# Kernel optimization log

Hardware: AMD Instinct MI355X
Metric: run time of the kernel (lower is better)

## Reference

```python
import jax, jax.numpy as jnp
import numpy as np

N_NODES = 50000
N_EDGES = 800000
NFEAT, NHID, ZDIM = 256, 128, 32
N_PAIRS = 10000


def spmm(row, col, val, h, n):
    # sparse adj (COO) @ dense h : gather source rows, scale, segment-sum into dest rows
    return jax.ops.segment_sum(val[:, None] * h[col], row, num_segments=n)


def setup_inputs() -> dict:
    key = jax.random.key(0)
    ks = jax.random.split(key, 16)
    features = jax.random.normal(ks[0], (N_NODES, NFEAT), dtype=jnp.float32)
    adj_row = jnp.sort(jax.random.randint(ks[1], (N_EDGES,), 0, N_NODES, dtype=jnp.int32))
    adj_col = jax.random.randint(ks[2], (N_EDGES,), 0, N_NODES, dtype=jnp.int32)
    adj_val = jax.random.uniform(ks[3], (N_EDGES,), dtype=jnp.float32)
    idx = jax.random.randint(ks[4], (2, N_PAIRS), 0, N_NODES, dtype=jnp.int32)
    sc = lambda fan: 1.0 / np.sqrt(fan)
    W0 = jax.random.normal(ks[5], (NFEAT, NHID), dtype=jnp.float32) * sc(NFEAT)
    b0 = jnp.zeros((NHID,), jnp.float32)
    W1 = jax.random.normal(ks[6], (NHID, NHID), dtype=jnp.float32) * sc(NHID)
    b1 = jnp.zeros((NHID,), jnp.float32)
    W2 = jax.random.normal(ks[7], (NHID, NHID), dtype=jnp.float32) * sc(NHID)
    b2 = jnp.zeros((NHID,), jnp.float32)
    bil_w = jax.random.normal(ks[8], (ZDIM, NHID, NHID), dtype=jnp.float32) * sc(NHID)
    bil_b = jnp.zeros((ZDIM,), jnp.float32)
    dw1 = jax.random.normal(ks[9], (ZDIM, ZDIM), dtype=jnp.float32) * sc(ZDIM)
    db1 = jnp.zeros((ZDIM,), jnp.float32)
    dw2 = jax.random.normal(ks[10], (ZDIM, 1), dtype=jnp.float32) * sc(ZDIM)
    db2 = jnp.zeros((1,), jnp.float32)
    return dict(features=features, adj_row=adj_row, adj_col=adj_col, adj_val=adj_val,
                idx=idx, W0=W0, b0=b0, W1=W1, b1=b1, W2=W2, b2=b2,
                bil_w=bil_w, bil_b=bil_b, dw1=dw1, db1=db1, dw2=dw2, db2=db2)


def reference(features, adj_row, adj_col, adj_val, idx,
              W0, b0, W1, b1, W2, b2, bil_w, bil_b, dw1, db1, dw2, db2):
    n = features.shape[0]
    # encode: stacked GCN layers (Kipf: relu(adj @ (x @ W) + b)), residual from layer 1 on
    x = jax.nn.relu(spmm(adj_row, adj_col, adj_val, features @ W0, n) + b0)
    res = x
    x = jax.nn.relu(spmm(adj_row, adj_col, adj_val, x @ W1, n) + b1) + res
    res = x
    x = jax.nn.relu(spmm(adj_row, adj_col, adj_val, x @ W2, n) + b2) + res
    latent = x  # dropout p=0.0 -> identity
    # decode: bilinear on node pairs, ELU, 2-layer MLP
    a = latent[idx[0]]  # [P, NHID]
    b = latent[idx[1]]  # [P, NHID]
    feat = jax.nn.elu(jnp.einsum('pd,kde,pe->pk', a, bil_w, b) + bil_b)
    h = jax.nn.elu(feat @ dw1 + db1)
    predictions = h @ dw2 + db2  # [P, 1]
    return predictions, latent
```

## Files before the change

### kernel.cpp

```cpp
#include <hip/hip_runtime.h>
#include <hip/hip_bf16.h>
#include <math.h>

#define N_NODES 50000
#define N_EDGES 800000
#define NFEAT   256
#define NHID    128
#define ZDIM    32
#define N_PAIRS 10000

typedef __attribute__((ext_vector_type(8))) short bf16x8;
typedef __attribute__((ext_vector_type(4))) float f32x4;

__global__ void k_build_row_ptr(const int* __restrict__ row, int* __restrict__ row_ptr) {
    int e = blockIdx.x * blockDim.x + threadIdx.x;
    if (e >= N_EDGES) return;
    int cur  = row[e];
    int prev = (e == 0) ? -1 : row[e - 1];
    for (int r = prev + 1; r <= cur; ++r) row_ptr[r] = e;
    if (e == N_EDGES - 1) {
        for (int r = cur + 1; r <= N_NODES; ++r) row_ptr[r] = N_EDGES;
    }
}

template <int K>
__global__ __launch_bounds__(256) void k_gemm(const float* __restrict__ X,
                                              const float* __restrict__ W,
                                              float* __restrict__ Y) {
    const int ROWS = 32;
    __shared__ float xs[ROWS][K];
    const int tid = threadIdx.x;
    const long r0 = (long)blockIdx.x * ROWS;

    const float4* X4 = reinterpret_cast<const float4*>(X + r0 * K);
    float4* xs4 = reinterpret_cast<float4*>(&xs[0][0]);
    const int NV = ROWS * K / 4;
    for (int i = tid; i < NV; i += 256) {
        int row = i / (K / 4);
        float4 v = make_float4(0.f, 0.f, 0.f, 0.f);
        if (r0 + row < N_NODES) v = X4[i];
        xs4[i] = v;
    }
    __syncthreads();

    const int cp = tid & 63;
    const int rbase = (tid >> 6) * 8;

    float acc[8][2];
#pragma unroll
    for (int r = 0; r < 8; ++r) { acc[r][0] = 0.f; acc[r][1] = 0.f; }

    for (int k = 0; k < K; k += 4) {
        float2 w0 = *reinterpret_cast<const float2*>(&W[(k + 0) * 128 + 2 * cp]);
        float2 w1 = *reinterpret_cast<const float2*>(&W[(k + 1) * 128 + 2 * cp]);
        float2 w2 = *reinterpret_cast<const float2*>(&W[(k + 2) * 128 + 2 * cp]);
        float2 w3 = *reinterpret_cast<const float2*>(&W[(k + 3) * 128 + 2 * cp]);
#pragma unroll
        for (int r = 0; r < 8; ++r) {
            float4 a = *reinterpret_cast<const float4*>(&xs[rbase + r][k]);
            acc[r][0] += a.x * w0.x + a.y * w1.x + a.z * w2.x + a.w * w3.x;
            acc[r][1] += a.x * w0.y + a.y * w1.y + a.z * w2.y + a.w * w3.y;
        }
    }
#pragma unroll
    for (int r = 0; r < 8; ++r) {
        long row = r0 + rbase + r;
        if (row < N_NODES)
            *reinterpret_cast<float2*>(&Y[row * 128 + 2 * cp]) = make_float2(acc[r][0], acc[r][1]);
    }
}

template <bool HAS_RES>
__global__ __launch_bounds__(256) void k_spmm_post(const float* __restrict__ H,
                                                   const int* __restrict__ row_ptr,
                                                   const int* __restrict__ col,
                                                   const float* __restrict__ val,
                                                   const float* __restrict__ bias,
                                                   const float* __restrict__ res,
                                                   float* __restrict__ out) {
    const int w    = threadIdx.x >> 6;
    const int lane = threadIdx.x & 63;
    const int r    = blockIdx.x * 4 + w;
    if (r >= N_NODES) return;
    const int e0 = row_ptr[r], e1 = row_ptr[r + 1];
    const float2* H2 = reinterpret_cast<const float2*>(H);

    float2 acc = make_float2(0.f, 0.f);
    for (int base = e0; base < e1; base += 64) {
        int n = e1 - base; if (n > 64) n = 64;
        float v = 0.f; int c = 0;
        if (lane < n) { v = val[base + lane]; c = col[base + lane]; }
#pragma unroll 2
        for (int i = 0; i < n; ++i) {
            float vi = __shfl(v, i);
            int   ci = __shfl(c, i);
            float2 h = H2[(long)ci * 64 + lane];
            acc.x += vi * h.x;
            acc.y += vi * h.y;
        }
    }

    float2 bv = reinterpret_cast<const float2*>(bias)[lane];
    acc.x = fmaxf(acc.x + bv.x, 0.f);
    acc.y = fmaxf(acc.y + bv.y, 0.f);
    if (HAS_RES) {
        float2 rv = reinterpret_cast<const float2*>(res)[(long)r * 64 + lane];
        acc.x += rv.x; acc.y += rv.y;
    }
    reinterpret_cast<float2*>(out)[(long)r * 64 + lane] = acc;
}

__global__ __launch_bounds__(256) void k_pack_w(const float* __restrict__ bw,
                                                __hip_bfloat16* __restrict__ wpk) {
    int i  = blockIdx.x * 256 + threadIdx.x;
    int j  = i & 7;
    int l  = (i >> 3) & 63;
    int n  = (i >> 9) & 7;
    int kk = (i >> 12) & 3;
    int k  = i >> 14;
    int d  = kk * 32 + (l >> 4) * 8 + j;
    int e  = n * 16 + (l & 15);
    wpk[i] = __float2bfloat16(bw[((long)k * 128 + d) * 128 + e]);
}

__global__ __launch_bounds__(512, 4) void k_bilinear_mfma(const float* __restrict__ latent,
                                                          const int* __restrict__ idx0,
                                                          const int* __restrict__ idx1,
                                                          const __hip_bfloat16* __restrict__ wpk,
                                                          const float* __restrict__ bb,
                                                          const float* __restrict__ dw1,
                                                          const float* __restrict__ db1,
                                                          const float* __restrict__ dw2,
                                                          const float* __restrict__ db2,
                                                          float* __restrict__ pred) {
    __shared__ __hip_bfloat16 as[32][136];
    __shared__ float          bs[32][132];
    __shared__ float          fl[ZDIM][32];
    const int p0  = blockIdx.x * 32;
    const int tid = threadIdx.x;

    for (int i = tid; i < 32 * 32; i += 512) {
        int p = i >> 5, q = i & 31;
        int pi = p0 + p; if (pi >= N_PAIRS) pi = N_PAIRS - 1;
        const float4 av = *reinterpret_cast<const float4*>(&latent[(long)idx0[pi] * 128 + q * 4]);
        const float4 bv = *reinterpret_cast<const float4*>(&latent[(long)idx1[pi] * 128 + q * 4]);
        as[p][q * 4 + 0] = __float2bfloat16(av.x);
        as[p][q * 4 + 1] = __float2bfloat16(av.y);
        as[p][q * 4 + 2] = __float2bfloat16(av.z);
        as[p][q * 4 + 3] = __float2bfloat16(av.w);
        *reinterpret_cast<float4*>(&bs[p][q * 4]) = bv;
    }
    __syncthreads();

    const int wave = tid >> 6;
    const int lane = tid & 63;
    const int l15  = lane & 15, l4 = lane >> 4;

    bf16x8 af[2][4];
#pragma unroll
    for (int M = 0; M < 2; ++M)
#pragma unroll
        for (int kk = 0; kk < 4; ++kk)
            af[M][kk] = *reinterpret_cast<const bf16x8*>(&as[M * 16 + l15][kk * 32 + l4 * 8]);

#pragma unroll 1
    for (int k2 = 0; k2 < 4; ++k2) {
        const int k = wave * 4 + k2;
        float fsum[2][4];
#pragma unroll
        for (int M = 0; M < 2; ++M)
#pragma unroll
            for (int q = 0; q < 4; ++q) fsum[M][q] = 0.f;

#pragma unroll 1
        for (int n = 0; n < 8; ++n) {
            f32x4 acc0 = {0.f, 0.f, 0.f, 0.f};
            f32x4 acc1 = {0.f, 0.f, 0.f, 0.f};
#pragma unroll
            for (int kk = 0; kk < 4; ++kk) {
                bf16x8 wf = *reinterpret_cast<const bf16x8*>(
                    &wpk[(((long)(k * 4 + kk) * 8 + n) * 512) + lane * 8]);
                acc0 = __builtin_amdgcn_mfma_f32_16x16x32_bf16(af[0][kk], wf, acc0, 0, 0, 0);
                acc1 = __builtin_amdgcn_mfma_f32_16x16x32_bf16(af[1][kk], wf, acc1, 0, 0, 0);
            }
#pragma unroll
            for (int q = 0; q < 4; ++q) {
                fsum[0][q] += acc0[q] * bs[l4 * 4 + q][n * 16 + l15];
                fsum[1][q] += acc1[q] * bs[16 + l4 * 4 + q][n * 16 + l15];
            }
        }

#pragma unroll
        for (int M = 0; M < 2; ++M) {
            float v0 = fsum[M][0], v1 = fsum[M][1], v2 = fsum[M][2], v3 = fsum[M][3];
#pragma unroll
            for (int off = 1; off < 16; off <<= 1) {
                v0 += __shfl_xor(v0, off);
                v1 += __shfl_xor(v1, off);
                v2 += __shfl_xor(v2, off);
                v3 += __shfl_xor(v3, off);
            }
            if (l15 == 0) {
                const float bbk = bb[k];
                float vv[4] = {v0, v1, v2, v3};
#pragma unroll
                for (int q = 0; q < 4; ++q) {
                    float v = vv[q] + bbk;
                    fl[k][M * 16 + l4 * 4 + q] = (v > 0.f) ? v : (expf(v) - 1.f);
                }
            }
        }
    }
    __syncthreads();

    if (tid < 32) {
        int p = p0 + tid;
        if (p < N_PAIRS) {
            float f[ZDIM];
#pragma unroll
            for (int k = 0; k < ZDIM; ++k) f[k] = fl[k][tid];
            float acc = db2[0];
            for (int j = 0; j < ZDIM; ++j) {
                float h = db1[j];
#pragma unroll
                for (int k = 0; k < ZDIM; ++k) h += f[k] * dw1[k * ZDIM + j];
                h = (h > 0.f) ? h : (expf(h) - 1.f);
                acc += h * dw2[j];
            }
            pred[p] = acc;
        }
    }
}

extern "C" void kernel_launch(void* const* d_in, const int* in_sizes, int n_in,
                              void* d_out, int out_size, void* d_ws, size_t ws_size,
                              hipStream_t stream) {
    const float* features = (const float*)d_in[0];
    const int*   adj_row  = (const int*)d_in[1];
    const int*   adj_col  = (const int*)d_in[2];
    const float* adj_val  = (const float*)d_in[3];
    const int*   idx      = (const int*)d_in[4];
    const float* W0 = (const float*)d_in[5];
    const float* b0 = (const float*)d_in[6];
    const float* W1 = (const float*)d_in[7];
    const float* b1 = (const float*)d_in[8];
    const float* W2 = (const float*)d_in[9];
    const float* b2 = (const float*)d_in[10];
    const float* bil_w = (const float*)d_in[11];
    const float* bil_b = (const float*)d_in[12];
    const float* dw1 = (const float*)d_in[13];
    const float* db1 = (const float*)d_in[14];
    const float* dw2 = (const float*)d_in[15];
    const float* db2 = (const float*)d_in[16];

    float* pred   = (float*)d_out;
    float* latent = (float*)d_out + N_PAIRS;

    char* ws = (char*)d_ws;
    float* xw   = (float*)ws;                                 ws += (size_t)N_NODES * NHID * 4;
    float* xcur = (float*)ws;                                 ws += (size_t)N_NODES * NHID * 4;
    int*   row_ptr = (int*)ws;                                ws += (size_t)(N_NODES + 1) * 4;
    __hip_bfloat16* wpk = (__hip_bfloat16*)ws;                ws += (size_t)ZDIM * NHID * NHID * 2;

    const int*  idx0 = idx;
    const int*  idx1 = idx + N_PAIRS;

    k_build_row_ptr<<<(N_EDGES + 255) / 256, 256, 0, stream>>>(adj_row, row_ptr);
    k_pack_w<<<(ZDIM * NHID * NHID) / 256, 256, 0, stream>>>(bil_w, wpk);

    const int GB  = (N_NODES + 31) / 32;
    const int SB  = (N_NODES + 3) / 4;

    k_gemm<NFEAT><<<GB, 256, 0, stream>>>(features, W0, xw);
    k_spmm_post<false><<<SB, 256, 0, stream>>>(xw, row_ptr, adj_col, adj_val, b0, nullptr, xcur);

    k_gemm<NHID><<<GB, 256, 0, stream>>>(xcur, W1, xw);
    k_spmm_post<true><<<SB, 256, 0, stream>>>(xw, row_ptr, adj_col, adj_val, b1, xcur, xcur);

    k_gemm<NHID><<<GB, 256, 0, stream>>>(xcur, W2, xw);
    k_spmm_post<true><<<SB, 256, 0, stream>>>(xw, row_ptr, adj_col, adj_val, b2, xcur, latent);

    k_bilinear_mfma<<<(N_PAIRS + 31) / 32, 512, 0, stream>>>(latent, idx0, idx1, wpk, bil_b,
                                                             dw1, db1, dw2, db2, pred);
}
```

Measured before the change: 496.6 us.

## Move node GEMMs to bf16 MFMA and split bilinear into hi/lo bf16 terms

Replaces the scalar FP32 feature GEMMs with bf16 MFMA kernels that take weights pre-packed into the MFMA fragment layout, 64 rows per block. The aim is to cut the VALU-bound cost of the three dense transforms. The bilinear decoder now splits activations and weights into high and low bf16 parts and issues three MFMAs per step instead of one, which recovers accuracy at the price of three times the MFMA work and extra loads. The node GEMMs themselves lose precision because their inputs are rounded to bf16.

```diff
diff --git a/kernel.cpp b/kernel.cpp
--- a/kernel.cpp
+++ b/kernel.cpp
@@ -23,51 +23,88 @@
     }
 }
 
+__global__ __launch_bounds__(256) void k_pack_gw(const float* __restrict__ W,
+                                                 __hip_bfloat16* __restrict__ wpk) {
+    int i  = blockIdx.x * 256 + threadIdx.x;
+    int j  = i & 7;
+    int l  = (i >> 3) & 63;
+    int n  = (i >> 9) & 7;
+    int kk = i >> 12;
+    int d  = kk * 32 + (l >> 4) * 8 + j;
+    int e  = n * 16 + (l & 15);
+    wpk[i] = __float2bfloat16(W[(long)d * 128 + e]);
+}
+
+__global__ __launch_bounds__(256) void k_pack_w2(const float* __restrict__ bw,
+                                                 __hip_bfloat16* __restrict__ wh,
+                                                 __hip_bfloat16* __restrict__ wl) {
+    int i  = blockIdx.x * 256 + threadIdx.x;
+    int j  = i & 7;
+    int l  = (i >> 3) & 63;
+    int n  = (i >> 9) & 7;
+    int kk = (i >> 12) & 3;
+    int k  = i >> 14;
+    int d  = kk * 32 + (l >> 4) * 8 + j;
+    int e  = n * 16 + (l & 15);
+    float w = bw[((long)k * 128 + d) * 128 + e];
+    __hip_bfloat16 h = __float2bfloat16(w);
+    wh[i] = h;
+    wl[i] = __float2bfloat16(w - __bfloat162float(h));
+}
+
 template <int K>
-__global__ __launch_bounds__(256) void k_gemm(const float* __restrict__ X,
-                                              const float* __restrict__ W,
-                                              float* __restrict__ Y) {
-    const int ROWS = 32;
-    __shared__ float xs[ROWS][K];
+__global__ __launch_bounds__(256) void k_gemm_mfma(const float* __restrict__ X,
+                                                   const __hip_bfloat16* __restrict__ wpk,
+                                                   float* __restrict__ Y) {
+    const int PAD = 8;
+    __shared__ __hip_bfloat16 as[64][K + PAD];
     const int tid = threadIdx.x;
-    const long r0 = (long)blockIdx.x * ROWS;
-
-    const float4* X4 = reinterpret_cast<const float4*>(X + r0 * K);
-    float4* xs4 = reinterpret_cast<float4*>(&xs[0][0]);
-    const int NV = ROWS * K / 4;
-    for (int i = tid; i < NV; i += 256) {
-        int row = i / (K / 4);
+    const long r0 = (long)blockIdx.x * 64;
+
+    const int QK = K / 4;
+    for (int i = tid; i < 64 * QK; i += 256) {
+        int row = i / QK, q = i - row * QK;
         float4 v = make_float4(0.f, 0.f, 0.f, 0.f);
-        if (r0 + row < N_NODES) v = X4[i];
-        xs4[i] = v;
+        if (r0 + row < N_NODES)
+            v = *reinterpret_cast<const float4*>(&X[(r0 + row) * (long)K + q * 4]);
+        as[row][q * 4 + 0] = __float2bfloat16(v.x);
+        as[row][q * 4 + 1] = __float2bfloat16(v.y);
+        as[row][q * 4 + 2] = __float2bfloat16(v.z);
+        as[row][q * 4 + 3] = __float2bfloat16(v.w);
     }
     __syncthreads();
 
-    const int cp = tid & 63;
-    const int rbase = (tid >> 6) * 8;
-
-    float acc[8][2];
-#pragma unroll
-    for (int r = 0; r < 8; ++r) { acc[r][0] = 0.f; acc[r][1] = 0.f; }
-
-    for (int k = 0; k < K; k += 4) {
-        float2 w0 = *reinterpret_cast<const float2*>(&W[(k + 0) * 128 + 2 * cp]);
-        float2 w1 = *reinterpret_cast<const float2*>(&W[(k + 1) * 128 + 2 * cp]);
-        float2 w2 = *reinterpret_cast<const float2*>(&W[(k + 2) * 128 + 2 * cp]);
-        float2 w3 = *reinterpret_cast<const float2*>(&W[(k + 3) * 128 + 2 * cp]);
-#pragma unroll
-        for (int r = 0; r < 8; ++r) {
-            float4 a = *reinterpret_cast<const float4*>(&xs[rbase + r][k]);
-            acc[r][0] += a.x * w0.x + a.y * w1.x + a.z * w2.x + a.w * w3.x;
-            acc[r][1] += a.x * w0.y + a.y * w1.y + a.z * w2.y + a.w * w3.y;
-        }
-    }
-#pragma unroll
-    for (int r = 0; r < 8; ++r) {
-        long row = r0 + rbase + r;
-        if (row < N_NODES)
-            *reinterpret_cast<float2*>(&Y[row * 128 + 2 * cp]) = make_float2(acc[r][0], acc[r][1]);
-    }
+    const int wrow = (tid >> 6) * 16;
+    const int lane = tid & 63;
+    const int l15  = lane & 15, l4 = lane >> 4;
+
+    bf16x8 af[K / 32];
+#pragma unroll
+    for (int kk = 0; kk < K / 32; ++kk)
+        af[kk] = *reinterpret_cast<const bf16x8*>(&as[wrow + l15][kk * 32 + l4 * 8]);
+
+    f32x4 acc[8];
+#pragma unroll
+    for (int n = 0; n < 8; ++n) acc[n] = (f32x4){0.f, 0.f, 0.f, 0.f};
+
+#pragma unroll 2
+    for (int n = 0; n < 8; ++n) {
+        f32x4 a = {0.f, 0.f, 0.f, 0.f};
+#pragma unroll
+        for (int kk = 0; kk < K / 32; ++kk) {
+            bf16x8 wf = *reinterpret_cast<const bf16x8*>(&wpk[(((kk * 8 + n) * 64) + lane) * 8]);
+            a = __builtin_amdgcn_mfma_f32_16x16x32_bf16(af[kk], wf, a, 0, 0, 0);
+        }
+        acc[n] = a;
+    }
+
+#pragma unroll
+    for (int n = 0; n < 8; ++n)
+#pragma unroll
+        for (int q = 0; q < 4; ++q) {
+            long row = r0 + wrow + l4 * 4 + q;
+            if (row < N_NODES) Y[row * 128 + n * 16 + l15] = acc[n][q];
+        }
 }
 
 template <bool HAS_RES>
@@ -110,30 +147,19 @@
     reinterpret_cast<float2*>(out)[(long)r * 64 + lane] = acc;
 }
 
-__global__ __launch_bounds__(256) void k_pack_w(const float* __restrict__ bw,
-                                                __hip_bfloat16* __restrict__ wpk) {
-    int i  = blockIdx.x * 256 + threadIdx.x;
-    int j  = i & 7;
-    int l  = (i >> 3) & 63;
-    int n  = (i >> 9) & 7;
-    int kk = (i >> 12) & 3;
-    int k  = i >> 14;
-    int d  = kk * 32 + (l >> 4) * 8 + j;
-    int e  = n * 16 + (l & 15);
-    wpk[i] = __float2bfloat16(bw[((long)k * 128 + d) * 128 + e]);
-}
-
 __global__ __launch_bounds__(512, 4) void k_bilinear_mfma(const float* __restrict__ latent,
                                                           const int* __restrict__ idx0,
                                                           const int* __restrict__ idx1,
-                                                          const __hip_bfloat16* __restrict__ wpk,
+                                                          const __hip_bfloat16* __restrict__ wpk_hi,
+                                                          const __hip_bfloat16* __restrict__ wpk_lo,
                                                           const float* __restrict__ bb,
                                                           const float* __restrict__ dw1,
                                                           const float* __restrict__ db1,
                                                           const float* __restrict__ dw2,
                                                           const float* __restrict__ db2,
                                                           float* __restrict__ pred) {
-    __shared__ __hip_bfloat16 as[32][136];
+    __shared__ __hip_bfloat16 ah[32][136];
+    __shared__ __hip_bfloat16 al[32][136];
     __shared__ float          bs[32][132];
     __shared__ float          fl[ZDIM][32];
     const int p0  = blockIdx.x * 32;
@@ -144,10 +170,13 @@
         int pi = p0 + p; if (pi >= N_PAIRS) pi = N_PAIRS - 1;
         const float4 av = *reinterpret_cast<const float4*>(&latent[(long)idx0[pi] * 128 + q * 4]);
         const float4 bv = *reinterpret_cast<const float4*>(&latent[(long)idx1[pi] * 128 + q * 4]);
-        as[p][q * 4 + 0] = __float2bfloat16(av.x);
-        as[p][q * 4 + 1] = __float2bfloat16(av.y);
-        as[p][q * 4 + 2] = __float2bfloat16(av.z);
-        as[p][q * 4 + 3] = __float2bfloat16(av.w);
+        float a4[4] = {av.x, av.y, av.z, av.w};
+#pragma unroll
+        for (int t = 0; t < 4; ++t) {
+            __hip_bfloat16 h = __float2bfloat16(a4[t]);
+            ah[p][q * 4 + t] = h;
+            al[p][q * 4 + t] = __float2bfloat16(a4[t] - __bfloat162float(h));
+        }
         *reinterpret_cast<float4*>(&bs[p][q * 4]) = bv;
     }
     __syncthreads();
@@ -161,7 +190,7 @@
     for (int M = 0; M < 2; ++M)
 #pragma unroll
         for (int kk = 0; kk < 4; ++kk)
-            af[M][kk] = *reinterpret_cast<const bf16x8*>(&as[M * 16 + l15][kk * 32 + l4 * 8]);
+            af[M][kk] = *reinterpret_cast<const bf16x8*>(&ah[M * 16 + l15][kk * 32 + l4 * 8]);
 
 #pragma unroll 1
     for (int k2 = 0; k2 < 4; ++k2) {
@@ -178,10 +207,17 @@
             f32x4 acc1 = {0.f, 0.f, 0.f, 0.f};
 #pragma unroll
             for (int kk = 0; kk < 4; ++kk) {
-                bf16x8 wf = *reinterpret_cast<const bf16x8*>(
-                    &wpk[(((long)(k * 4 + kk) * 8 + n) * 512) + lane * 8]);
-                acc0 = __builtin_amdgcn_mfma_f32_16x16x32_bf16(af[0][kk], wf, acc0, 0, 0, 0);
-                acc1 = __builtin_amdgcn_mfma_f32_16x16x32_bf16(af[1][kk], wf, acc1, 0, 0, 0);
+                const long ci = (((long)(k * 4 + kk) * 8 + n) * 512) + lane * 8;
+                bf16x8 wh = *reinterpret_cast<const bf16x8*>(&wpk_hi[ci]);
+                bf16x8 wl = *reinterpret_cast<const bf16x8*>(&wpk_lo[ci]);
+                bf16x8 a0l = *reinterpret_cast<const bf16x8*>(&al[l15][kk * 32 + l4 * 8]);
+                bf16x8 a1l = *reinterpret_cast<const bf16x8*>(&al[16 + l15][kk * 32 + l4 * 8]);
+                acc0 = __builtin_amdgcn_mfma_f32_16x16x32_bf16(af[0][kk], wh, acc0, 0, 0, 0);
+                acc0 = __builtin_amdgcn_mfma_f32_16x16x32_bf16(af[0][kk], wl, acc0, 0, 0, 0);
+                acc0 = __builtin_amdgcn_mfma_f32_16x16x32_bf16(a0l,      wh, acc0, 0, 0, 0);
+                acc1 = __builtin_amdgcn_mfma_f32_16x16x32_bf16(af[1][kk], wh, acc1, 0, 0, 0);
+                acc1 = __builtin_amdgcn_mfma_f32_16x16x32_bf16(af[1][kk], wl, acc1, 0, 0, 0);
+                acc1 = __builtin_amdgcn_mfma_f32_16x16x32_bf16(a1l,      wh, acc1, 0, 0, 0);
             }
 #pragma unroll
             for (int q = 0; q < 4; ++q) {
@@ -260,26 +296,33 @@
     float* xw   = (float*)ws;                                 ws += (size_t)N_NODES * NHID * 4;
     float* xcur = (float*)ws;                                 ws += (size_t)N_NODES * NHID * 4;
     int*   row_ptr = (int*)ws;                                ws += (size_t)(N_NODES + 1) * 4;
-    __hip_bfloat16* wpk = (__hip_bfloat16*)ws;                ws += (size_t)ZDIM * NHID * NHID * 2;
+    __hip_bfloat16* wpk_hi = (__hip_bfloat16*)ws;             ws += (size_t)ZDIM * NHID * NHID * 2;
+    __hip_bfloat16* wpk_lo = (__hip_bfloat16*)ws;             ws += (size_t)ZDIM * NHID * NHID * 2;
+    __hip_bfloat16* w0pk = (__hip_bfloat16*)ws;               ws += (size_t)NFEAT * NHID * 2;
+    __hip_bfloat16* w1pk = (__hip_bfloat16*)ws;               ws += (size_t)NHID * NHID * 2;
+    __hip_bfloat16* w2pk = (__hip_bfloat16*)ws;               ws += (size_t)NHID * NHID * 2;
 
     const int*  idx0 = idx;
     const int*  idx1 = idx + N_PAIRS;
 
     k_build_row_ptr<<<(N_EDGES + 255) / 256, 256, 0, stream>>>(adj_row, row_ptr);
-    k_pack_w<<<(ZDIM * NHID * NHID) / 256, 256, 0, stream>>>(bil_w, wpk);
-
-    const int GB  = (N_NODES + 31) / 32;
+    k_pack_w2<<<(ZDIM * NHID * NHID) / 256, 256, 0, stream>>>(bil_w, wpk_hi, wpk_lo);
+    k_pack_gw<<<(NFEAT * NHID) / 256, 256, 0, stream>>>(W0, w0pk);
+    k_pack_gw<<<(NHID * NHID) / 256, 256, 0, stream>>>(W1, w1pk);
+    k_pack_gw<<<(NHID * NHID) / 256, 256, 0, stream>>>(W2, w2pk);
+
+    const int GB  = (N_NODES + 63) / 64;
     const int SB  = (N_NODES + 3) / 4;
 
-    k_gemm<NFEAT><<<GB, 256, 0, stream>>>(features, W0, xw);
+    k_gemm_mfma<NFEAT><<<GB, 256, 0, stream>>>(features, w0pk, xw);
     k_spmm_post<false><<<SB, 256, 0, stream>>>(xw, row_ptr, adj_col, adj_val, b0, nullptr, xcur);
 
-    k_gemm<NHID><<<GB, 256, 0, stream>>>(xcur, W1, xw);
+    k_gemm_mfma<NHID><<<GB, 256, 0, stream>>>(xcur, w1pk, xw);
     k_spmm_post<true><<<SB, 256, 0, stream>>>(xw, row_ptr, adj_col, adj_val, b1, xcur, xcur);
 
-    k_gemm<NHID><<<GB, 256, 0, stream>>>(xcur, W2, xw);
+    k_gemm_mfma<NHID><<<GB, 256, 0, stream>>>(xcur, w2pk, xw);
     k_spmm_post<true><<<SB, 256, 0, stream>>>(xw, row_ptr, adj_col, adj_val, b2, xcur, latent);
 
-    k_bilinear_mfma<<<(N_PAIRS + 31) / 32, 512, 0, stream>>>(latent, idx0, idx1, wpk, bil_b,
-                                                             dw1, db1, dw2, db2, pred);
-}
+    k_bilinear_mfma<<<(N_PAIRS + 31) / 32, 512, 0, stream>>>(latent, idx0, idx1, wpk_hi, wpk_lo,
+                                                             bil_b, dw1, db1, dw2, db2, pred);
+}
```

Measured after the change: 431.2 us. 13.2% less time.
